# Kernel tuning notes

Measured on AMD Instinct MI355X. Metric: run time of the kernel, lower is better.

## Reference

```python
import jax, jax.numpy as jnp
import numpy as np

N_NODES = 50000
N_EDGES = 800000
D = 128


def gcn_conv(x, src, dst, W, b, n):
    # PyG GCNConv: h = x @ W; add self-loops; symmetric normalization
    # D^{-1/2} (A + I) D^{-1/2}; aggregate at destination; add bias.
    loop = jnp.arange(n, dtype=src.dtype)
    s = jnp.concatenate([src, loop])
    d = jnp.concatenate([dst, loop])
    deg = jax.ops.segment_sum(jnp.ones_like(d, dtype=x.dtype), d, num_segments=n)
    dinv = jnp.where(deg > 0, jax.lax.rsqrt(deg), 0.0)
    norm = dinv[s] * dinv[d]  # [E+N]
    h = x @ W                  # [N, hidden]
    msg = norm[:, None] * h[s]  # gather -> [E+N, hidden]
    out = jax.ops.segment_sum(msg, d, num_segments=n)  # scatter-add
    return out + b


def setup_inputs() -> dict:
    key = jax.random.key(0)
    ks = jax.random.split(key, 6)
    x = jax.random.normal(ks[0], (N_NODES, D), dtype=jnp.float32)
    edge_index = jax.random.randint(ks[1], (2, N_EDGES), 0, N_NODES, dtype=jnp.int32)
    sc = 1.0 / np.sqrt(D)
    W1 = jax.random.normal(ks[2], (D, D), dtype=jnp.float32) * sc
    b1 = jnp.zeros((D,), dtype=jnp.float32)
    W2 = jax.random.normal(ks[3], (D, D), dtype=jnp.float32) * sc
    b2 = jnp.zeros((D,), dtype=jnp.float32)
    lin_W = jax.random.normal(ks[4], (2 * D, D), dtype=jnp.float32) * (1.0 / np.sqrt(2 * D))
    lin_b = jnp.zeros((D,), dtype=jnp.float32)
    return {"x": x, "edge_index": edge_index, "W1": W1, "b1": b1,
            "W2": W2, "b2": b2, "lin_W": lin_W, "lin_b": lin_b}


def reference(x, edge_index, W1, b1, W2, b2, lin_W, lin_b):
    n = x.shape[0]
    src, dst = edge_index[0], edge_index[1]
    x1 = jax.nn.relu(gcn_conv(x, src, dst, W1, b1, n))
    x2 = jax.nn.relu(gcn_conv(x1, src, dst, W2, b2, n))
    jk = jnp.concatenate([x1, x2], axis=-1)  # JumpingKnowledge 'cat'
    return jk @ lin_W + lin_b
```

## Files before the change

kernel.cpp:

```cpp
#include <hip/hip_runtime.h>


#define D128 128

typedef __attribute__((ext_vector_type(8))) short bf16x8;
typedef __attribute__((ext_vector_type(4))) float f32x4;

__device__ __forceinline__ unsigned short f2bf_bits(float v) {
    unsigned int u = __float_as_uint(v);
    unsigned int r = u + 0x7FFFu + ((u >> 16) & 1u);
    return (unsigned short)(r >> 16);
}
__device__ __forceinline__ float bflo(unsigned int u) { return __uint_as_float(u << 16); }
__device__ __forceinline__ float bfhi(unsigned int u) { return __uint_as_float(u & 0xFFFF0000u); }

__global__ void k_count(const int* __restrict__ dst, int* __restrict__ indeg, int E) {
    int base = (blockIdx.x * 256 + threadIdx.x) * 4;
    if (base + 3 < E) {
        int4 d = *(const int4*)&dst[base];
        atomicAdd(&indeg[d.x], 1);
        atomicAdd(&indeg[d.y], 1);
        atomicAdd(&indeg[d.z], 1);
        atomicAdd(&indeg[d.w], 1);
    } else {
        for (int e = base; e < E; ++e) atomicAdd(&indeg[dst[e]], 1);
    }
}

__global__ void k_scan1(const int* __restrict__ indeg, int* __restrict__ row_ptr,
                        int* __restrict__ bsum, float* __restrict__ dinv, int n) {
    __shared__ int tmp[256];
    int i = blockIdx.x * 256 + threadIdx.x;
    int v = (i < n) ? indeg[i] : 0;
    if (i < n) dinv[i] = rsqrtf((float)(v + 1));
    tmp[threadIdx.x] = v;
    __syncthreads();
    for (int off = 1; off < 256; off <<= 1) {
        int t = (threadIdx.x >= off) ? tmp[threadIdx.x - off] : 0;
        __syncthreads();
        tmp[threadIdx.x] += t;
        __syncthreads();
    }
    if (i < n) row_ptr[i] = tmp[threadIdx.x] - v;
    if (threadIdx.x == 255) bsum[blockIdx.x] = tmp[255];
}

__global__ void k_scan23(int* __restrict__ row_ptr, const int* __restrict__ bsum,
                         int* __restrict__ cursor, int n, int E, int nb) {
    __shared__ int tmp[256];
    __shared__ int exc[256];
    int t = threadIdx.x;
    int v = (t < nb) ? bsum[t] : 0;
    tmp[t] = v;
    __syncthreads();
    for (int off = 1; off < 256; off <<= 1) {
        int x = (t >= off) ? tmp[t - off] : 0;
        __syncthreads();
        tmp[t] += x;
        __syncthreads();
    }
    exc[t] = tmp[t] - v;
    __syncthreads();
    int add = exc[blockIdx.x];
    int i = blockIdx.x * 256 + t;
    if (i < n) {
        int r = row_ptr[i] + add;
        row_ptr[i] = r;
        cursor[i] = r;
    }
    if (blockIdx.x == 0 && t == 0) row_ptr[n] = E;
}

__global__ __launch_bounds__(256) void k_agg_csr(
    const unsigned int* __restrict__ h, const int* __restrict__ row_ptr,
    const int* __restrict__ csr_src, const float* __restrict__ dinv,
    const float* __restrict__ bias, float* __restrict__ o, int n)
{
    int node = blockIdx.x * 4 + (threadIdx.x >> 6);
    int lane = threadIdx.x & 63;
    if (node >= n) return;
    float dv = dinv[node];
    unsigned int su = h[node * 64 + lane];
    float ax = dv * bflo(su);
    float ay = dv * bfhi(su);
    int j = row_ptr[node], end = row_ptr[node + 1];
    for (; j + 7 < end; j += 8) {
        int s0 = csr_src[j+0], s1 = csr_src[j+1], s2 = csr_src[j+2], s3 = csr_src[j+3];
        int s4 = csr_src[j+4], s5 = csr_src[j+5], s6 = csr_src[j+6], s7 = csr_src[j+7];
        float d0 = dinv[s0], d1 = dinv[s1], d2 = dinv[s2], d3 = dinv[s3];
        float d4 = dinv[s4], d5 = dinv[s5], d6 = dinv[s6], d7 = dinv[s7];
        unsigned int u0 = h[s0 * 64 + lane];
        unsigned int u1 = h[s1 * 64 + lane];
        unsigned int u2 = h[s2 * 64 + lane];
        unsigned int u3 = h[s3 * 64 + lane];
        unsigned int u4 = h[s4 * 64 + lane];
        unsigned int u5 = h[s5 * 64 + lane];
        unsigned int u6 = h[s6 * 64 + lane];
        unsigned int u7 = h[s7 * 64 + lane];
        ax += d0*bflo(u0) + d1*bflo(u1) + d2*bflo(u2) + d3*bflo(u3)
            + d4*bflo(u4) + d5*bflo(u5) + d6*bflo(u6) + d7*bflo(u7);
        ay += d0*bfhi(u0) + d1*bfhi(u1) + d2*bfhi(u2) + d3*bfhi(u3)
            + d4*bfhi(u4) + d5*bfhi(u5) + d6*bfhi(u6) + d7*bfhi(u7);
    }
    for (; j + 3 < end; j += 4) {
        int s0 = csr_src[j+0], s1 = csr_src[j+1], s2 = csr_src[j+2], s3 = csr_src[j+3];
        float d0 = dinv[s0], d1 = dinv[s1], d2 = dinv[s2], d3 = dinv[s3];
        unsigned int u0 = h[s0 * 64 + lane];
        unsigned int u1 = h[s1 * 64 + lane];
        unsigned int u2 = h[s2 * 64 + lane];
        unsigned int u3 = h[s3 * 64 + lane];
        ax += d0*bflo(u0) + d1*bflo(u1) + d2*bflo(u2) + d3*bflo(u3);
        ay += d0*bfhi(u0) + d1*bfhi(u1) + d2*bfhi(u2) + d3*bfhi(u3);
    }
    for (; j < end; ++j) {
        int s = csr_src[j];
        float d = dinv[s];
        unsigned int u = h[s * 64 + lane];
        ax += d * bflo(u);
        ay += d * bfhi(u);
    }
    float2 bv = ((const float2*)bias)[lane];
    float2 ov = {fmaxf(dv * ax + bv.x, 0.f), fmaxf(dv * ay + bv.y, 0.f)};
    ((float2*)o)[node * 64 + lane] = ov;
}

__device__ __forceinline__ void stage_A_tile(
    const float* __restrict__ A, int brow, int n, int tid,
    unsigned short* __restrict__ Ah)
{
    const float4* A4 = (const float4*)(A + (size_t)brow * D128);
#pragma unroll
    for (int it = 0; it < 8; ++it) {
        int f = it * 256 + tid;
        int r = f >> 5, k4 = f & 31;
        float4 v = make_float4(0.f, 0.f, 0.f, 0.f);
        if (brow + r < n) v = A4[f];
        int lane_ = (r & 15) + 16 * ((k4 >> 1) & 3);
        int base = ((((k4 >> 3) * 4 + (r >> 4)) * 64 + lane_) << 3) + (k4 & 1) * 4;
        ushort4 hh;
        unsigned short* hp = (unsigned short*)&hh;
        hp[0] = f2bf_bits(v.x); hp[1] = f2bf_bits(v.y);
        hp[2] = f2bf_bits(v.z); hp[3] = f2bf_bits(v.w);
        *(ushort4*)&Ah[base] = hh;
    }
}

__device__ __forceinline__ void load_W_s(
    const float* __restrict__ W, int s, int colbase, int lanen, int kb,
    bf16x8 wh[2])
{
#pragma unroll
    for (int t = 0; t < 2; ++t)
#pragma unroll
        for (int j = 0; j < 8; ++j)
            wh[t][j] = (short)f2bf_bits(W[(size_t)(s * 32 + kb + j) * D128 + colbase + t * 16 + lanen]);
}

__device__ __forceinline__ void epilogue(
    f32x4 acc[4][2], float* __restrict__ C, const float* __restrict__ bias,
    int brow, int n, int colbase, int lanen, int l, int out_bf, int addC)
{
    float bv[2] = {0.f, 0.f};
    if (bias) { bv[0] = bias[colbase + lanen]; bv[1] = bias[colbase + 16 + lanen]; }
    int rsub = (l >> 4) * 4;
    if (out_bf) {
        unsigned short* Cb = (unsigned short*)C;
#pragma unroll
        for (int m = 0; m < 4; ++m)
#pragma unroll
            for (int t = 0; t < 2; ++t)
#pragma unroll
                for (int r = 0; r < 4; ++r) {
                    int row = brow + m * 16 + rsub + r;
                    if (row < n)
                        Cb[(size_t)row * D128 + colbase + t * 16 + lanen] = f2bf_bits(acc[m][t][r]);
                }
    } else {
#pragma unroll
        for (int m = 0; m < 4; ++m)
#pragma unroll
            for (int t = 0; t < 2; ++t)
#pragma unroll
                for (int r = 0; r < 4; ++r) {
                    int row = brow + m * 16 + rsub + r;
                    if (row < n) {
                        size_t idx = (size_t)row * D128 + colbase + t * 16 + lanen;
                        float v = acc[m][t][r] + bv[t];
                        if (addC) v += C[idx];
                        C[idx] = v;
                    }
                }
    }
}

__device__ __forceinline__ void gemm_core(
    const float* __restrict__ A, const float* __restrict__ W,
    const float* __restrict__ bias, float* __restrict__ C,
    int n, int out_bf, int addC, int bid, int tid,
    unsigned short* __restrict__ Ah)
{
    int l = tid & 63;
    int wv = tid >> 6;
    int brow = bid * 64;
    int colbase = wv * 32;
    int lanen = l & 15;
    int kb = (l >> 4) * 8;

    f32x4 acc[4][2];
#pragma unroll
    for (int m = 0; m < 4; ++m)
#pragma unroll
        for (int t = 0; t < 2; ++t) acc[m][t] = (f32x4){0.f, 0.f, 0.f, 0.f};

    stage_A_tile(A, brow, n, tid, Ah);
    __syncthreads();

#pragma unroll
    for (int s = 0; s < 4; ++s) {
        bf16x8 wh[2];
        load_W_s(W, s, colbase, lanen, kb, wh);
#pragma unroll
        for (int m = 0; m < 4; ++m) {
            bf16x8 ah = *(const bf16x8*)&Ah[((s * 4 + m) * 64 + l) * 8];
#pragma unroll
            for (int t = 0; t < 2; ++t)
                acc[m][t] = __builtin_amdgcn_mfma_f32_16x16x32_bf16(ah, wh[t], acc[m][t], 0, 0, 0);
        }
    }
    epilogue(acc, C, bias, brow, n, colbase, lanen, l, out_bf, addC);
}

__global__ __launch_bounds__(256, 2) void k_gemm1_fill(
    const float* __restrict__ x, const float* __restrict__ W1,
    float* __restrict__ h, int n,
    const int* __restrict__ src, const int* __restrict__ dst,
    int* __restrict__ cursor, int* __restrict__ csr_src,
    int E, int gemmBlocks)
{
    __shared__ unsigned short Ah[4 * 4 * 64 * 8];
    if (blockIdx.x < gemmBlocks) {
        gemm_core(x, W1, nullptr, h, n, 1, 0, blockIdx.x, threadIdx.x, Ah);
    } else {
        int e = (blockIdx.x - gemmBlocks) * 256 + threadIdx.x;
        if (e >= E) return;
        int s = src[e], d = dst[e];
        int pos = atomicAdd(&cursor[d], 1);
        csr_src[pos] = s;
    }
}

__global__ __launch_bounds__(256, 2) void k_gemm_mfma(
    const float* __restrict__ A, const float* __restrict__ W,
    const float* __restrict__ bias, float* __restrict__ C,
    int n, int out_bf, int addC)
{
    __shared__ unsigned short Ah[4 * 4 * 64 * 8];
    gemm_core(A, W, bias, C, n, out_bf, addC, blockIdx.x, threadIdx.x, Ah);
}

__global__ __launch_bounds__(256, 2) void k_gemm_dual(
    const float* __restrict__ A, const float* __restrict__ W2,
    const float* __restrict__ Wtop, float* __restrict__ hOut,
    float* __restrict__ pOut, int n)
{
    __shared__ unsigned short Ah[4 * 4 * 64 * 8];
    int tid = threadIdx.x;
    int l = tid & 63;
    int wv = tid >> 6;
    int brow = blockIdx.x * 64;
    int colbase = wv * 32;
    int lanen = l & 15;
    int kb = (l >> 4) * 8;

    f32x4 accA[4][2], accB[4][2];
#pragma unroll
    for (int m = 0; m < 4; ++m)
#pragma unroll
        for (int t = 0; t < 2; ++t) {
            accA[m][t] = (f32x4){0.f, 0.f, 0.f, 0.f};
            accB[m][t] = (f32x4){0.f, 0.f, 0.f, 0.f};
        }

    stage_A_tile(A, brow, n, tid, Ah);
    __syncthreads();

#pragma unroll
    for (int s = 0; s < 4; ++s) {
        bf16x8 whA[2], whB[2];
        load_W_s(W2, s, colbase, lanen, kb, whA);
        load_W_s(Wtop, s, colbase, lanen, kb, whB);
#pragma unroll
        for (int m = 0; m < 4; ++m) {
            bf16x8 ah = *(const bf16x8*)&Ah[((s * 4 + m) * 64 + l) * 8];
#pragma unroll
            for (int t = 0; t < 2; ++t) {
                accA[m][t] = __builtin_amdgcn_mfma_f32_16x16x32_bf16(ah, whA[t], accA[m][t], 0, 0, 0);
                accB[m][t] = __builtin_amdgcn_mfma_f32_16x16x32_bf16(ah, whB[t], accB[m][t], 0, 0, 0);
            }
        }
    }
    epilogue(accA, hOut, nullptr, brow, n, colbase, lanen, l, 1, 0);
    epilogue(accB, pOut, nullptr, brow, n, colbase, lanen, l, 0, 0);
}

extern "C" void kernel_launch(void* const* d_in, const int* in_sizes, int n_in,
                              void* d_out, int out_size, void* d_ws, size_t ws_size,
                              hipStream_t stream) {
    const float* x    = (const float*)d_in[0];
    const int*   ei   = (const int*)d_in[1];
    const float* W1   = (const float*)d_in[2];
    const float* b1   = (const float*)d_in[3];
    const float* W2   = (const float*)d_in[4];
    const float* b2   = (const float*)d_in[5];
    const float* linW = (const float*)d_in[6];
    const float* linb = (const float*)d_in[7];

    int n = in_sizes[0] / D128;
    int E = in_sizes[1] / 2;
    const int* src = ei;
    const int* dst = ei + E;

    float* out = (float*)d_out;
    float* ws  = (float*)d_ws;

    size_t o = 0;
    int*   csr_src = (int*)(ws + o);    o += E;
    int*   indeg   = (int*)(ws + o);    o += n;
    float* dinv    = ws + o;            o += n;
    int*   row_ptr = (int*)(ws + o);    o += n + 1;
    int*   bsum    = (int*)(ws + o);    o += 256;
    int*   cursor  = (int*)(ws + o);    o += n;
    o = (o + 3) & ~(size_t)3;
    float* x1      = ws + o;            o += (size_t)n * D128;
    float* x2      = ws + o;            o += (size_t)n * D128;
    float* h       = ws + o;

    int gn = (n + 255) / 256;
    int gE  = (E + 255) / 256;
    int gE4 = (E + 1023) / 1024;
    int gemmBlocks = (n + 63) / 64;
    int aggBlocks  = (n + 3) / 4;

    (void)hipMemsetAsync(indeg, 0, (size_t)n * sizeof(int), stream);
    k_count<<<gE4, 256, 0, stream>>>(dst, indeg, E);
    k_scan1<<<gn, 256, 0, stream>>>(indeg, row_ptr, bsum, dinv, n);
    k_scan23<<<gn, 256, 0, stream>>>(row_ptr, bsum, cursor, n, E, gn);

    k_gemm1_fill<<<gemmBlocks + gE, 256, 0, stream>>>(
        x, W1, h, n, src, dst, cursor, csr_src, E, gemmBlocks);

    k_agg_csr<<<aggBlocks, 256, 0, stream>>>((const unsigned int*)h, row_ptr, csr_src, dinv, b1, x1, n);

    k_gemm_dual<<<gemmBlocks, 256, 0, stream>>>(x1, W2, linW, h, out, n);

    k_agg_csr<<<aggBlocks, 256, 0, stream>>>((const unsigned int*)h, row_ptr, csr_src, dinv, b2, x2, n);

    k_gemm_mfma<<<gemmBlocks, 256, 0, stream>>>(x2, linW + 128 * D128, linb, out, n, 0, 1);
}
```

Baseline: 232.7 us.

## Split CSR aggregation into feature-column phases with edge-parallel lanes

The aggregation kernel now launches four phases, each covering 16 of the 64 packed bf16-pair columns. Each wavefront splits into four 16-lane slots that gather different neighbor edges in parallel, and the partial sums are combined with cross-lane shuffles. The aim is more parallel independent gathers per wavefront and, with phases in separate block ranges, a smaller per-phase working set of h columns for better cache locality. In exchange, the CSR indices and dinv values are re-read once per phase, rows touched per edge drop to 64-byte segments, and the launch has four times as many blocks.

```diff
diff --git a/kernel.cpp b/kernel.cpp
--- a/kernel.cpp
+++ b/kernel.cpp
@@ -2,6 +2,7 @@
 
 
 #define D128 128
+#define NPHASE 4
 
 typedef __attribute__((ext_vector_type(8))) short bf16x8;
 typedef __attribute__((ext_vector_type(4))) float f32x4;
@@ -71,57 +72,57 @@
     if (blockIdx.x == 0 && t == 0) row_ptr[n] = E;
 }
 
-__global__ __launch_bounds__(256) void k_agg_csr(
+__global__ __launch_bounds__(256) void k_agg_phase(
     const unsigned int* __restrict__ h, const int* __restrict__ row_ptr,
     const int* __restrict__ csr_src, const float* __restrict__ dinv,
-    const float* __restrict__ bias, float* __restrict__ o, int n)
-{
-    int node = blockIdx.x * 4 + (threadIdx.x >> 6);
+    const float* __restrict__ bias, float* __restrict__ o, int n, int ngroups)
+{
+    int phase = blockIdx.x / ngroups;
+    int grp   = blockIdx.x % ngroups;
+    int node  = grp * 4 + (threadIdx.x >> 6);
+    if (node >= n) return;
     int lane = threadIdx.x & 63;
-    if (node >= n) return;
-    float dv = dinv[node];
-    unsigned int su = h[node * 64 + lane];
-    float ax = dv * bflo(su);
-    float ay = dv * bfhi(su);
+    int slot = lane >> 4;
+    int ci   = lane & 15;
+    int hoff = phase * 16 + ci;
+
+    float ax = 0.f, ay = 0.f;
     int j = row_ptr[node], end = row_ptr[node + 1];
-    for (; j + 7 < end; j += 8) {
-        int s0 = csr_src[j+0], s1 = csr_src[j+1], s2 = csr_src[j+2], s3 = csr_src[j+3];
-        int s4 = csr_src[j+4], s5 = csr_src[j+5], s6 = csr_src[j+6], s7 = csr_src[j+7];
+    for (; j + 15 < end; j += 16) {
+        int s0 = csr_src[j + slot];
+        int s1 = csr_src[j + 4 + slot];
+        int s2 = csr_src[j + 8 + slot];
+        int s3 = csr_src[j + 12 + slot];
         float d0 = dinv[s0], d1 = dinv[s1], d2 = dinv[s2], d3 = dinv[s3];
-        float d4 = dinv[s4], d5 = dinv[s5], d6 = dinv[s6], d7 = dinv[s7];
-        unsigned int u0 = h[s0 * 64 + lane];
-        unsigned int u1 = h[s1 * 64 + lane];
-        unsigned int u2 = h[s2 * 64 + lane];
-        unsigned int u3 = h[s3 * 64 + lane];
-        unsigned int u4 = h[s4 * 64 + lane];
-        unsigned int u5 = h[s5 * 64 + lane];
-        unsigned int u6 = h[s6 * 64 + lane];
-        unsigned int u7 = h[s7 * 64 + lane];
-        ax += d0*bflo(u0) + d1*bflo(u1) + d2*bflo(u2) + d3*bflo(u3)
-            + d4*bflo(u4) + d5*bflo(u5) + d6*bflo(u6) + d7*bflo(u7);
-        ay += d0*bfhi(u0) + d1*bfhi(u1) + d2*bfhi(u2) + d3*bfhi(u3)
-            + d4*bfhi(u4) + d5*bfhi(u5) + d6*bfhi(u6) + d7*bfhi(u7);
-    }
-    for (; j + 3 < end; j += 4) {
-        int s0 = csr_src[j+0], s1 = csr_src[j+1], s2 = csr_src[j+2], s3 = csr_src[j+3];
-        float d0 = dinv[s0], d1 = dinv[s1], d2 = dinv[s2], d3 = dinv[s3];
-        unsigned int u0 = h[s0 * 64 + lane];
-        unsigned int u1 = h[s1 * 64 + lane];
-        unsigned int u2 = h[s2 * 64 + lane];
-        unsigned int u3 = h[s3 * 64 + lane];
+        unsigned int u0 = h[(size_t)s0 * 64 + hoff];
+        unsigned int u1 = h[(size_t)s1 * 64 + hoff];
+        unsigned int u2 = h[(size_t)s2 * 64 + hoff];
+        unsigned int u3 = h[(size_t)s3 * 64 + hoff];
         ax += d0*bflo(u0) + d1*bflo(u1) + d2*bflo(u2) + d3*bflo(u3);
         ay += d0*bfhi(u0) + d1*bfhi(u1) + d2*bfhi(u2) + d3*bfhi(u3);
     }
-    for (; j < end; ++j) {
-        int s = csr_src[j];
-        float d = dinv[s];
-        unsigned int u = h[s * 64 + lane];
+    for (; j < end; j += 4) {
+        int e = j + slot;
+        int ee = (e < end) ? e : (end - 1);
+        int s = csr_src[ee];
+        float d = (e < end) ? dinv[s] : 0.f;
+        unsigned int u = h[(size_t)s * 64 + hoff];
         ax += d * bflo(u);
         ay += d * bfhi(u);
     }
-    float2 bv = ((const float2*)bias)[lane];
-    float2 ov = {fmaxf(dv * ax + bv.x, 0.f), fmaxf(dv * ay + bv.y, 0.f)};
-    ((float2*)o)[node * 64 + lane] = ov;
+
+    ax += __shfl_xor(ax, 16); ay += __shfl_xor(ay, 16);
+    ax += __shfl_xor(ax, 32); ay += __shfl_xor(ay, 32);
+
+    if (slot == 0) {
+        float dv = dinv[node];
+        unsigned int su = h[(size_t)node * 64 + hoff];
+        ax += dv * bflo(su);
+        ay += dv * bfhi(su);
+        float2 bv = ((const float2*)bias)[hoff];
+        float2 ov = {fmaxf(dv * ax + bv.x, 0.f), fmaxf(dv * ay + bv.y, 0.f)};
+        ((float2*)o)[(size_t)node * 64 + hoff] = ov;
+    }
 }
 
 __device__ __forceinline__ void stage_A_tile(
@@ -339,7 +340,8 @@
     int gE  = (E + 255) / 256;
     int gE4 = (E + 1023) / 1024;
     int gemmBlocks = (n + 63) / 64;
-    int aggBlocks  = (n + 3) / 4;
+    int ngroups = (n + 3) / 4;
+    int aggBlocks = NPHASE * ngroups;
 
     (void)hipMemsetAsync(indeg, 0, (size_t)n * sizeof(int), stream);
     k_count<<<gE4, 256, 0, stream>>>(dst, indeg, E);
@@ -349,11 +351,11 @@
     k_gemm1_fill<<<gemmBlocks + gE, 256, 0, stream>>>(
         x, W1, h, n, src, dst, cursor, csr_src, E, gemmBlocks);
 
-    k_agg_csr<<<aggBlocks, 256, 0, stream>>>((const unsigned int*)h, row_ptr, csr_src, dinv, b1, x1, n);
+    k_agg_phase<<<aggBlocks, 256, 0, stream>>>((const unsigned int*)h, row_ptr, csr_src, dinv, b1, x1, n, ngroups);
 
     k_gemm_dual<<<gemmBlocks, 256, 0, stream>>>(x1, W2, linW, h, out, n);
 
-    k_agg_csr<<<aggBlocks, 256, 0, stream>>>((const unsigned int*)h, row_ptr, csr_src, dinv, b2, x2, n);
+    k_agg_phase<<<aggBlocks, 256, 0, stream>>>((const unsigned int*)h, row_ptr, csr_src, dinv, b2, x2, n, ngroups);
 
     k_gemm_mfma<<<gemmBlocks, 256, 0, stream>>>(x2, linW + 128 * D128, linb, out, n, 0, 1);
 }
```

Result: slower. 343.6 us (+47.7%).
